# Performance work log

Hardware: AMD Instinct MI355X
Metric: run time of the kernel (lower is better)

## Reference

```python
import jax, jax.numpy as jnp
import numpy as np

N, E, H, F, G, L = 20000, 320000, 128, 128, 50, 6
CUTOFF = 5.0
LOG2 = 0.6931471805599453  # shift of ShiftedSoftplus
PI = np.pi


def ssp(x):
    # ShiftedSoftplus: softplus(x) - log(2)
    return jax.nn.softplus(x) - LOG2


def setup_inputs() -> dict:
    key = jax.random.key(0)
    ks = jax.random.split(key, 12)
    v = jax.random.normal(ks[0], (N, H), jnp.float32)
    pos = jax.random.uniform(ks[1], (N, 3), jnp.float32) * 2.0
    offsets_real = jax.random.normal(ks[2], (E, 3), jnp.float32) * 0.3
    edges = jax.random.randint(ks[3], (2, E), 0, N, jnp.int32)
    s = lambda k, shp, fan_in: jax.random.normal(k, shp, jnp.float32) / np.sqrt(fan_in)
    # update_e params (torch Linear weights stored as [in, out] for x @ W)
    lin_w = s(ks[4], (L, H, F), H)        # Linear(hidden, filters, bias=False)
    w1 = s(ks[5], (L, G, F), G)           # mlp[0]: Linear(gaussians, filters)
    b1 = jnp.zeros((L, F), jnp.float32)
    w2 = s(ks[6], (L, F, F), F)           # mlp[2]: Linear(filters, filters)
    b2 = jnp.zeros((L, F), jnp.float32)
    # update_v params
    u1 = s(ks[7], (L, F, H), F)           # lin1: Linear(filters, hidden)
    ub1 = jnp.zeros((L, H), jnp.float32)
    u2 = s(ks[8], (L, H, H), H)           # lin2: Linear(hidden, hidden)
    ub2 = jnp.zeros((L, H), jnp.float32)
    return {"v": v, "pos": pos, "offsets_real": offsets_real, "edges": edges,
            "lin_w": lin_w, "w1": w1, "b1": b1, "w2": w2, "b2": b2,
            "u1": u1, "ub1": ub1, "u2": u2, "ub2": ub2}


def reference(v, pos, offsets_real, edges, lin_w, w1, b1, w2, b2, u1, ub1, u2, ub2):
    row, col = edges[0], edges[1]
    # pairwise distances with periodic offsets: [E]
    diff = pos[col] + offsets_real - pos[row]
    dist = jnp.sqrt(jnp.sum(diff * diff, axis=-1))
    # Gaussian RBF expansion: [E, G]
    offset = jnp.linspace(0.0, CUTOFF, G)
    coeff = -0.5 / (offset[1] - offset[0]) ** 2
    demb = jnp.exp(coeff * (dist[:, None] - offset[None, :]) ** 2)
    # cosine cutoff envelope: [E]
    C = 0.5 * (jnp.cos(dist * PI / CUTOFF) + 1.0)
    for l in range(L):
        # continuous filter from RBFs: [E, F]
        Wf = (ssp(demb @ w1[l] + b1[l]) @ w2[l] + b2[l]) * C[:, None]
        # update_e: project nodes then gather source features
        e = (v @ lin_w[l])[row] * Wf                      # [E, F]
        # update_v: scatter-add messages to targets, residual MLP
        agg = jax.ops.segment_sum(e, col, num_segments=N)  # [N, F]
        out = ssp(agg @ u1[l] + ub1[l]) @ u2[l] + ub2[l]
        v = v + out
    return v
```

## Files before the change

kernel.cpp:

```cpp
#include <hip/hip_runtime.h>
#include <hip/hip_bf16.h>
#include <math.h>

#define HH 128
#define FF 128
#define GG 50
#define NLAYERS 6
#define NPB 16
#define TAB 4096
#define TABH 0.001953125f
#define TABINVH 512.0f
#define SCB 32
#define DP 8

typedef __attribute__((ext_vector_type(8))) short bf16x8;
typedef __attribute__((ext_vector_type(4))) float f32x4;

static __device__ __forceinline__ float ssp(float x) {
    return fmaxf(x, 0.f) + __logf(1.f + __expf(-fabsf(x))) - 0.6931471805599453f;
}

static __device__ __forceinline__ short f2bf(float x) {
    union { float f; unsigned u; } c; c.f = x;
    unsigned r = (c.u + 0x7FFF + ((c.u >> 16) & 1)) >> 16;
    return (short)r;
}

static __device__ __forceinline__ float bf2f_lo(unsigned p) {
    union { unsigned u; float f; } c; c.u = p << 16; return c.f;
}
static __device__ __forceinline__ float bf2f_hi(unsigned p) {
    union { unsigned u; float f; } c; c.u = p & 0xFFFF0000u; return c.f;
}

__global__ void hist_kernel(const int* __restrict__ col, int* __restrict__ counts, int E_) {
    int e = blockIdx.x * 256 + threadIdx.x;
    if (e < E_) atomicAdd(&counts[col[e]], 1);
}

__global__ __launch_bounds__(1024) void pscan1_kernel(const int* __restrict__ counts,
                                                      int* __restrict__ psum, int N_) {
    __shared__ int wsum[16];
    const int tid = threadIdx.x;
    const int lane = tid & 63, wid = tid >> 6;
    const int chunk = (N_ + SCB - 1) / SCB;
    int i = blockIdx.x * chunk + tid;
    int val = (tid < chunk && i < N_) ? counts[i] : 0;
#pragma unroll
    for (int d = 1; d < 64; d <<= 1) val += __shfl_xor(val, d, 64);
    if (lane == 0) wsum[wid] = val;
    __syncthreads();
    if (wid == 0) {
        int s = (lane < 16) ? wsum[lane] : 0;
#pragma unroll
        for (int d = 1; d < 16; d <<= 1) s += __shfl_xor(s, d, 64);
        if (lane == 0) psum[blockIdx.x] = s;
    }
}

__global__ void pscan2_kernel(const int* __restrict__ psum, int* __restrict__ pbase) {
    const int tid = threadIdx.x;
    int v = (tid < SCB) ? psum[tid] : 0;
    int x = v;
#pragma unroll
    for (int d = 1; d < 64; d <<= 1) {
        int t = __shfl_up(x, d, 64);
        if (tid >= d) x += t;
    }
    if (tid < SCB) pbase[tid] = x - v;
}

__global__ __launch_bounds__(1024) void pscan3_kernel(const int* __restrict__ counts,
                                                      const int* __restrict__ pbase,
                                                      int* __restrict__ offsets,
                                                      int* __restrict__ woff, int N_) {
    __shared__ int wsum[16];
    const int tid = threadIdx.x;
    const int lane = tid & 63, wid = tid >> 6;
    const int chunk = (N_ + SCB - 1) / SCB;
    int i = blockIdx.x * chunk + tid;
    int val = (tid < chunk && i < N_) ? counts[i] : 0;
    int x = val;
#pragma unroll
    for (int d = 1; d < 64; d <<= 1) {
        int t = __shfl_up(x, d, 64);
        if (lane >= d) x += t;
    }
    if (lane == 63) wsum[wid] = x;
    __syncthreads();
    if (wid == 0) {
        int s = (lane < 16) ? wsum[lane] : 0;
#pragma unroll
        for (int d = 1; d < 16; d <<= 1) {
            int t = __shfl_up(s, d, 64);
            if (lane >= d) s += t;
        }
        if (lane < 16) wsum[lane] = s;
    }
    __syncthreads();
    int woffset = (wid > 0) ? wsum[wid - 1] : 0;
    if (tid < chunk && i < N_) {
        int ex = pbase[blockIdx.x] + woffset + x - val;
        offsets[i] = ex;
        woff[i] = ex;
    }
}

__global__ void scatter_kernel(const float* __restrict__ pos,
                               const float* __restrict__ offs,
                               const int* __restrict__ row,
                               const int* __restrict__ col,
                               int* __restrict__ woff,
                               int2* __restrict__ meta, int E_) {
    int e = blockIdx.x * 256 + threadIdx.x;
    if (e >= E_) return;
    int r = row[e], c = col[e];
    float dx = pos[c * 3 + 0] + offs[e * 3 + 0] - pos[r * 3 + 0];
    float dy = pos[c * 3 + 1] + offs[e * 3 + 1] - pos[r * 3 + 1];
    float dz = pos[c * 3 + 2] + offs[e * 3 + 2] - pos[r * 3 + 2];
    float d = sqrtf(dx * dx + dy * dy + dz * dz);
    float x = d * TABINVH;
    int ix = (int)x;
    if (ix > TAB - 2) ix = TAB - 2;
    float fr = x - (float)ix;
    unsigned frb = (unsigned)(unsigned short)f2bf(fr);
    int p = atomicAdd(&woff[c], 1);
    meta[p] = make_int2(r, (int)((frb << 16) | (unsigned)ix));
}

__global__ __launch_bounds__(256) void prep_kernel(
    const float* __restrict__ w1, const float* __restrict__ w2,
    const float* __restrict__ u1, const float* __restrict__ u2,
    const float* __restrict__ lin_w,
    short* __restrict__ w1t, short* __restrict__ w2t,
    short* __restrict__ u1t, short* __restrict__ u2t, short* __restrict__ lin_wt) {
    int idx = blockIdx.x * 256 + threadIdx.x;
    if (idx < NLAYERS * FF * FF) {
        int l = idx >> 14, r = idx & 16383, a = r >> 7, b = r & 127;
        size_t src = (size_t)l * FF * FF + (size_t)b * FF + a;
        w2t[idx] = f2bf(w2[src]);
        u1t[idx] = f2bf(u1[src]);
        u2t[idx] = f2bf(u2[src]);
        lin_wt[idx] = f2bf(lin_w[src]);
    }
    if (idx < NLAYERS * FF * 64) {
        int l = idx >> 13, r = idx & 8191, fo = r >> 6, g = r & 63;
        w1t[idx] = f2bf(g < GG ? w1[((size_t)l * GG + g) * FF + fo] : 0.f);
    }
}

__global__ __launch_bounds__(256) void vproj0_kernel(const float* __restrict__ vb,
                                                     const short* __restrict__ lwt,
                                                     unsigned short* __restrict__ out,
                                                     int N_) {
    const int tid = threadIdx.x;
    const int lane = tid & 63, wave = tid >> 6;
    const int l15 = lane & 15, l4 = lane >> 4;
    const int n0 = wave * 32;
    const int nb0 = blockIdx.x * 64;
    bf16x8 bw[2][4];
#pragma unroll
    for (int n = 0; n < 2; n++)
#pragma unroll
        for (int ks = 0; ks < 4; ks++)
            bw[n][ks] = *(const bf16x8*)&lwt[(n0 + n * 16 + l15) * 128 + ks * 32 + l4 * 8];
#pragma unroll
    for (int m = 0; m < 4; m++) {
        f32x4 acc0 = {0.f, 0.f, 0.f, 0.f}, acc1 = {0.f, 0.f, 0.f, 0.f};
        int arow = nb0 + m * 16 + l15;
        const float* ap = &vb[(size_t)(arow < N_ ? arow : 0) * HH];
#pragma unroll
        for (int ks = 0; ks < 4; ks++) {
            float4 x0 = *(const float4*)&ap[ks * 32 + l4 * 8];
            float4 x1 = *(const float4*)&ap[ks * 32 + l4 * 8 + 4];
            bf16x8 a = {f2bf(x0.x), f2bf(x0.y), f2bf(x0.z), f2bf(x0.w),
                        f2bf(x1.x), f2bf(x1.y), f2bf(x1.z), f2bf(x1.w)};
            acc0 = __builtin_amdgcn_mfma_f32_16x16x32_bf16(a, bw[0][ks], acc0, 0, 0, 0);
            acc1 = __builtin_amdgcn_mfma_f32_16x16x32_bf16(a, bw[1][ks], acc1, 0, 0, 0);
        }
#pragma unroll
        for (int r = 0; r < 4; r++) {
            int gn = nb0 + m * 16 + l4 * 4 + r;
            if (gn < N_) {
                out[(size_t)gn * FF + n0 + l15] = (unsigned short)f2bf(acc0[r]);
                out[(size_t)gn * FF + n0 + 16 + l15] = (unsigned short)f2bf(acc1[r]);
            }
        }
    }
}

__global__ __launch_bounds__(256) void tab_kernel(
    const short* __restrict__ w1t, const float* __restrict__ b1,
    const short* __restrict__ w2t, const float* __restrict__ b2,
    unsigned short* __restrict__ tab) {
    __shared__ __align__(16) short h1_s[64 * 136];
    const int tid = threadIdx.x;
    const int lane = tid & 63, wave = tid >> 6;
    const int l15 = lane & 15, l4 = lane >> 4;
    const int n0w = wave * 32;
    const int l = blockIdx.x / (TAB / 64);
    const int tb0 = (blockIdx.x % (TAB / 64)) * 64;
    const short* w1l = w1t + (size_t)l * FF * 64;
    const short* w2l = w2t + (size_t)l * FF * FF;
    unsigned short* tabl = tab + (size_t)l * TAB * FF;

    bf16x8 bw1[2][2], bw2[2][4];
    float bias1[2], bias2[2];
#pragma unroll
    for (int n = 0; n < 2; n++) {
        const int fo = n0w + n * 16 + l15;
        bias1[n] = b1[(size_t)l * FF + fo];
        bias2[n] = b2[(size_t)l * FF + fo];
#pragma unroll
        for (int ks = 0; ks < 2; ks++)
            bw1[n][ks] = *(const bf16x8*)&w1l[fo * 64 + ks * 32 + l4 * 8];
#pragma unroll
        for (int ks = 0; ks < 4; ks++)
            bw2[n][ks] = *(const bf16x8*)&w2l[fo * 128 + ks * 32 + l4 * 8];
    }

    const float STEP = 5.0f / 49.0f;
    const float COEFF = -0.5f / (STEP * STEP);
#pragma unroll
    for (int m = 0; m < 4; m++) {
        float d = (float)(tb0 + m * 16 + l15) * TABH;
        bf16x8 a0, a1;
#pragma unroll
        for (int j = 0; j < 8; j++) {
            int g0 = l4 * 8 + j;
            float x0 = fmaf((float)g0, -STEP, d);
            a0[j] = f2bf(__expf(COEFF * x0 * x0));
            int g1 = 32 + l4 * 8 + j;
            float x1 = fmaf((float)g1, -STEP, d);
            a1[j] = (g1 < GG) ? f2bf(__expf(COEFF * x1 * x1)) : (short)0;
        }
#pragma unroll
        for (int n = 0; n < 2; n++) {
            f32x4 acc = {bias1[n], bias1[n], bias1[n], bias1[n]};
            acc = __builtin_amdgcn_mfma_f32_16x16x32_bf16(a0, bw1[n][0], acc, 0, 0, 0);
            acc = __builtin_amdgcn_mfma_f32_16x16x32_bf16(a1, bw1[n][1], acc, 0, 0, 0);
            const int f = n0w + n * 16 + l15;
#pragma unroll
            for (int r = 0; r < 4; r++)
                h1_s[(m * 16 + l4 * 4 + r) * 136 + f] = f2bf(ssp(acc[r]));
        }
    }
    __syncthreads();

#pragma unroll
    for (int m = 0; m < 4; m++) {
        f32x4 accA = {bias2[0], bias2[0], bias2[0], bias2[0]};
        f32x4 accB = {bias2[1], bias2[1], bias2[1], bias2[1]};
#pragma unroll
        for (int ks = 0; ks < 4; ks++) {
            bf16x8 a = *(const bf16x8*)&h1_s[(m * 16 + l15) * 136 + ks * 32 + l4 * 8];
            accA = __builtin_amdgcn_mfma_f32_16x16x32_bf16(a, bw2[0][ks], accA, 0, 0, 0);
            accB = __builtin_amdgcn_mfma_f32_16x16x32_bf16(a, bw2[1][ks], accB, 0, 0, 0);
        }
#pragma unroll
        for (int r = 0; r < 4; r++) {
            int entry = tb0 + m * 16 + l4 * 4 + r;
            float de = (float)entry * TABH;
            float C = 0.5f * (cosf(de * 0.6283185307179586f) + 1.0f);
            tabl[(size_t)entry * FF + n0w + l15] = (unsigned short)f2bf(accA[r] * C);
            tabl[(size_t)entry * FF + n0w + 16 + l15] = (unsigned short)f2bf(accB[r] * C);
        }
    }
}

__global__ __launch_bounds__(256) void repack_kernel(const unsigned short* __restrict__ tab,
                                                     int2* __restrict__ tabp) {
    int idx = blockIdx.x * 256 + threadIdx.x;
    if (idx >= NLAYERS * TAB * 64) return;
    int l = idx / (TAB * 64);
    int r = idx - l * (TAB * 64);
    int i = r >> 6, f2 = r & 63;
    const unsigned short* tl = tab + (size_t)l * TAB * FF;
    unsigned lo = *(const unsigned*)&tl[(size_t)i * FF + 2 * f2];
    unsigned hi = (i + 1 < TAB) ? *(const unsigned*)&tl[(size_t)(i + 1) * FF + 2 * f2] : lo;
    tabp[idx] = make_int2((int)lo, (int)hi);
}

__global__ __launch_bounds__(512) void layer_kernel(
    const int2* __restrict__ meta,
    const int* __restrict__ off_start, const int* __restrict__ off_end,
    const int2* __restrict__ tabp, const unsigned* __restrict__ vin,
    const short* __restrict__ u1t, const float* __restrict__ ub1,
    const short* __restrict__ u2t, const float* __restrict__ ub2,
    float* __restrict__ vb, const short* __restrict__ lwt_next,
    unsigned short* __restrict__ vout, int N_) {
    __shared__ __align__(16) float agg_s[NPB * 132];
    __shared__ __align__(16) short t1_s[NPB * 136];
    short* t2_s = (short*)agg_s;

    const int tid = threadIdx.x;
    const int lane = tid & 63, wave = tid >> 6;
    const int l15 = lane & 15, l4 = lane >> 4;
    const int n0c = wave * 16;
    const int nb0 = blockIdx.x * NPB;

#pragma unroll
    for (int s = 0; s < 2; s++) {
        const int nl = wave * 2 + s;
        const int n = nb0 + nl;
        float acc0 = 0.f, acc1 = 0.f;
        if (n < N_) {
            const int e0 = __builtin_amdgcn_readfirstlane(off_start[n]);
            const int e1 = __builtin_amdgcn_readfirstlane(off_end[n]);
            if (e1 > e0) {
                int2 mmn[DP];
#pragma unroll
                for (int j = 0; j < DP; j++) {
                    int e = e0 + j; if (e >= e1) e = e1 - 1;
                    mmn[j] = meta[e];
                }
                for (int base = e0; base < e1; base += DP) {
                    int rr[DP], ww[DP];
#pragma unroll
                    for (int j = 0; j < DP; j++) {
                        rr[j] = __builtin_amdgcn_readfirstlane(mmn[j].x);
                        ww[j] = __builtin_amdgcn_readfirstlane(mmn[j].y);
                    }
                    int2 tp[DP]; unsigned vp[DP];
#pragma unroll
                    for (int j = 0; j < DP; j++) {
                        tp[j] = tabp[(size_t)(ww[j] & 0xffff) * 64 + lane];
                        vp[j] = vin[(size_t)rr[j] * 64 + lane];
                    }
                    const int nb2 = base + DP;
                    if (nb2 < e1) {
#pragma unroll
                        for (int j = 0; j < DP; j++) {
                            int e = nb2 + j; if (e >= e1) e = e1 - 1;
                            mmn[j] = meta[e];
                        }
                    }
#pragma unroll
                    for (int j = 0; j < DP; j++) {
                        if (base + j < e1) {
                            const float fr = bf2f_hi((unsigned)ww[j]);
                            const float ta0 = bf2f_lo((unsigned)tp[j].x);
                            const float ta1 = bf2f_hi((unsigned)tp[j].x);
                            const float tb0 = bf2f_lo((unsigned)tp[j].y);
                            const float tb1 = bf2f_hi((unsigned)tp[j].y);
                            acc0 = fmaf(fmaf(fr, tb0 - ta0, ta0), bf2f_lo(vp[j]), acc0);
                            acc1 = fmaf(fmaf(fr, tb1 - ta1, ta1), bf2f_hi(vp[j]), acc1);
                        }
                    }
                }
            }
        }
        agg_s[nl * 132 + 2 * lane] = acc0;
        agg_s[nl * 132 + 2 * lane + 1] = acc1;
    }
    __syncthreads();

    {
        bf16x8 bw[4];
        const float bias = ub1[n0c + l15];
#pragma unroll
        for (int ks = 0; ks < 4; ks++)
            bw[ks] = *(const bf16x8*)&u1t[(n0c + l15) * 128 + ks * 32 + l4 * 8];
        const float* ap = &agg_s[l15 * 132];
        f32x4 acc = {bias, bias, bias, bias};
#pragma unroll
        for (int ks = 0; ks < 4; ks++) {
            float4 x0 = *(const float4*)&ap[ks * 32 + l4 * 8];
            float4 x1 = *(const float4*)&ap[ks * 32 + l4 * 8 + 4];
            bf16x8 a = {f2bf(x0.x), f2bf(x0.y), f2bf(x0.z), f2bf(x0.w),
                        f2bf(x1.x), f2bf(x1.y), f2bf(x1.z), f2bf(x1.w)};
            acc = __builtin_amdgcn_mfma_f32_16x16x32_bf16(a, bw[ks], acc, 0, 0, 0);
        }
#pragma unroll
        for (int r = 0; r < 4; r++) {
            int er = l4 * 4 + r;
            t1_s[er * 136 + n0c + l15] = f2bf(ssp(acc[r]));
        }
    }
    __syncthreads();

    {
        bf16x8 bw[4];
        const float bias = ub2[n0c + l15];
#pragma unroll
        for (int ks = 0; ks < 4; ks++)
            bw[ks] = *(const bf16x8*)&u2t[(n0c + l15) * 128 + ks * 32 + l4 * 8];
        f32x4 acc = {bias, bias, bias, bias};
#pragma unroll
        for (int ks = 0; ks < 4; ks++) {
            bf16x8 a = *(const bf16x8*)&t1_s[(l15) * 136 + ks * 32 + l4 * 8];
            acc = __builtin_amdgcn_mfma_f32_16x16x32_bf16(a, bw[ks], acc, 0, 0, 0);
        }
        __syncthreads();
#pragma unroll
        for (int r = 0; r < 4; r++) {
            int er = l4 * 4 + r;
            int gn = nb0 + er;
            if (gn < N_) {
                size_t i0 = (size_t)gn * HH + n0c + l15;
                float v0 = vb[i0] + acc[r];
                vb[i0] = v0;
                t2_s[er * 136 + n0c + l15] = f2bf(v0);
            } else {
                t2_s[er * 136 + n0c + l15] = 0;
            }
        }
    }
    __syncthreads();

    if (lwt_next) {
        bf16x8 bw[4];
#pragma unroll
        for (int ks = 0; ks < 4; ks++)
            bw[ks] = *(const bf16x8*)&lwt_next[(n0c + l15) * 128 + ks * 32 + l4 * 8];
        f32x4 acc = {0.f, 0.f, 0.f, 0.f};
#pragma unroll
        for (int ks = 0; ks < 4; ks++) {
            bf16x8 a = *(const bf16x8*)&t2_s[(l15) * 136 + ks * 32 + l4 * 8];
            acc = __builtin_amdgcn_mfma_f32_16x16x32_bf16(a, bw[ks], acc, 0, 0, 0);
        }
#pragma unroll
        for (int r = 0; r < 4; r++) {
            int gn = nb0 + l4 * 4 + r;
            if (gn < N_) {
                vout[(size_t)gn * FF + n0c + l15] = (unsigned short)f2bf(acc[r]);
            }
        }
    }
}

extern "C" void kernel_launch(void* const* d_in, const int* in_sizes, int n_in,
                              void* d_out, int out_size, void* d_ws, size_t ws_size,
                              hipStream_t stream) {
    const float* v = (const float*)d_in[0];
    const float* pos = (const float*)d_in[1];
    const float* offs = (const float*)d_in[2];
    const int* edges = (const int*)d_in[3];
    const float* lin_w = (const float*)d_in[4];
    const float* w1 = (const float*)d_in[5];
    const float* b1 = (const float*)d_in[6];
    const float* w2 = (const float*)d_in[7];
    const float* b2 = (const float*)d_in[8];
    const float* u1 = (const float*)d_in[9];
    const float* ub1 = (const float*)d_in[10];
    const float* u2 = (const float*)d_in[11];
    const float* ub2 = (const float*)d_in[12];

    const int N = in_sizes[0] / HH;
    const int E = in_sizes[3] / 2;
    const int* row = edges;
    const int* col = edges + E;

    char* base = (char*)d_ws;
    int* counts = (int*)base;    base += (size_t)N * 4;
    int* woff = (int*)base;      base += (size_t)N * 4;
    int* offsets = (int*)base;   base += (size_t)N * 4;
    int* psum = (int*)base;      base += (size_t)SCB * 4;
    int* pbase = (int*)base;     base += (size_t)SCB * 4 + 24;
    int2* meta = (int2*)base;    base += (size_t)E * 8;
    unsigned short* vprojA = (unsigned short*)base; base += (size_t)N * FF * 2;
    unsigned short* vprojB = (unsigned short*)base; base += (size_t)N * FF * 2;
    short* w1t = (short*)base;   base += (size_t)NLAYERS * FF * 64 * 2;
    short* w2t = (short*)base;   base += (size_t)NLAYERS * FF * FF * 2;
    short* u1t = (short*)base;   base += (size_t)NLAYERS * FF * FF * 2;
    short* u2t = (short*)base;   base += (size_t)NLAYERS * FF * FF * 2;
    short* lin_wt = (short*)base; base += (size_t)NLAYERS * FF * FF * 2;
    unsigned short* tab = (unsigned short*)base; base += (size_t)NLAYERS * TAB * FF * 2;
    int2* tabp = (int2*)base;

    float* vbuf = (float*)d_out;

    const int EB = (E + 255) / 256;
    const int NB64 = (N + 63) / 64;
    const int NBn = (N + NPB - 1) / NPB;

    hipMemsetAsync(counts, 0, (size_t)N * 4, stream);
    hist_kernel<<<EB, 256, 0, stream>>>(col, counts, E);
    pscan1_kernel<<<SCB, 1024, 0, stream>>>(counts, psum, N);
    pscan2_kernel<<<1, 64, 0, stream>>>(psum, pbase);
    pscan3_kernel<<<SCB, 1024, 0, stream>>>(counts, pbase, offsets, woff, N);
    scatter_kernel<<<EB, 256, 0, stream>>>(pos, offs, row, col, woff, meta, E);
    prep_kernel<<<(NLAYERS * FF * FF + 255) / 256, 256, 0, stream>>>(
        w1, w2, u1, u2, lin_w, w1t, w2t, u1t, u2t, lin_wt);
    tab_kernel<<<NLAYERS * (TAB / 64), 256, 0, stream>>>(w1t, b1, w2t, b2, tab);
    repack_kernel<<<(NLAYERS * TAB * 64 + 255) / 256, 256, 0, stream>>>(tab, tabp);
    hipMemcpyAsync(vbuf, v, (size_t)N * HH * sizeof(float),
                   hipMemcpyDeviceToDevice, stream);
    vproj0_kernel<<<NB64, 256, 0, stream>>>(v, lin_wt, vprojA, N);

    for (int l = 0; l < NLAYERS; l++) {
        unsigned short* vin = (l & 1) ? vprojB : vprojA;
        unsigned short* vout = (l & 1) ? vprojA : vprojB;
        layer_kernel<<<NBn, 512, 0, stream>>>(
            meta, offsets, woff, tabp + (size_t)l * TAB * 64, (const unsigned*)vin,
            u1t + (size_t)l * FF * FF, ub1 + (size_t)l * HH,
            u2t + (size_t)l * FF * FF, ub2 + (size_t)l * HH, vbuf,
            (l + 1 < NLAYERS) ? (lin_wt + (size_t)(l + 1) * FF * FF) : nullptr,
            vout, N);
    }
}
```

Measured before the change: 310.2 us.

## Replace interpolated filter table with finer nearest-neighbor table and packed edge metadata

The filter lookup table grows 4x finer and uses nearest-entry lookup in place of linear interpolation. This removes the repack kernel and halves the per-edge table load from an int2 pair to one 32-bit word. Edge metadata is packed into a single int (17-bit row index plus table index), which halves metadata traffic, and the gather prefetch depth doubles. In exchange, the table build does 4x more MFMA work, the table gets larger and is less cache-friendly, and nearest-neighbor lookup adds some approximation error. The 17-bit row packing also assumes N stays below 131072.

```diff
diff --git a/kernel.cpp b/kernel.cpp
--- a/kernel.cpp
+++ b/kernel.cpp
@@ -7,11 +7,11 @@
 #define GG 50
 #define NLAYERS 6
 #define NPB 16
-#define TAB 4096
-#define TABH 0.001953125f
-#define TABINVH 512.0f
+#define TAB 16384
+#define TABH 4.8828125e-4f
+#define TABINVH 2048.0f
 #define SCB 32
-#define DP 8
+#define DP 16
 
 typedef __attribute__((ext_vector_type(8))) short bf16x8;
 typedef __attribute__((ext_vector_type(4))) float f32x4;
@@ -111,7 +111,7 @@
                                const int* __restrict__ row,
                                const int* __restrict__ col,
                                int* __restrict__ woff,
-                               int2* __restrict__ meta, int E_) {
+                               int* __restrict__ meta, int E_) {
     int e = blockIdx.x * 256 + threadIdx.x;
     if (e >= E_) return;
     int r = row[e], c = col[e];
@@ -119,13 +119,10 @@
     float dy = pos[c * 3 + 1] + offs[e * 3 + 1] - pos[r * 3 + 1];
     float dz = pos[c * 3 + 2] + offs[e * 3 + 2] - pos[r * 3 + 2];
     float d = sqrtf(dx * dx + dy * dy + dz * dz);
-    float x = d * TABINVH;
-    int ix = (int)x;
-    if (ix > TAB - 2) ix = TAB - 2;
-    float fr = x - (float)ix;
-    unsigned frb = (unsigned)(unsigned short)f2bf(fr);
+    int ix = (int)(d * TABINVH + 0.5f);
+    if (ix > TAB - 1) ix = TAB - 1;
     int p = atomicAdd(&woff[c], 1);
-    meta[p] = make_int2(r, (int)((frb << 16) | (unsigned)ix));
+    meta[p] = r | (ix << 17);
 }
 
 __global__ __launch_bounds__(256) void prep_kernel(
@@ -268,23 +265,10 @@
     }
 }
 
-__global__ __launch_bounds__(256) void repack_kernel(const unsigned short* __restrict__ tab,
-                                                     int2* __restrict__ tabp) {
-    int idx = blockIdx.x * 256 + threadIdx.x;
-    if (idx >= NLAYERS * TAB * 64) return;
-    int l = idx / (TAB * 64);
-    int r = idx - l * (TAB * 64);
-    int i = r >> 6, f2 = r & 63;
-    const unsigned short* tl = tab + (size_t)l * TAB * FF;
-    unsigned lo = *(const unsigned*)&tl[(size_t)i * FF + 2 * f2];
-    unsigned hi = (i + 1 < TAB) ? *(const unsigned*)&tl[(size_t)(i + 1) * FF + 2 * f2] : lo;
-    tabp[idx] = make_int2((int)lo, (int)hi);
-}
-
 __global__ __launch_bounds__(512) void layer_kernel(
-    const int2* __restrict__ meta,
+    const int* __restrict__ meta,
     const int* __restrict__ off_start, const int* __restrict__ off_end,
-    const int2* __restrict__ tabp, const unsigned* __restrict__ vin,
+    const unsigned* __restrict__ tab, const unsigned* __restrict__ vin,
     const short* __restrict__ u1t, const float* __restrict__ ub1,
     const short* __restrict__ u2t, const float* __restrict__ ub2,
     float* __restrict__ vb, const short* __restrict__ lwt_next,
@@ -308,24 +292,24 @@
             const int e0 = __builtin_amdgcn_readfirstlane(off_start[n]);
             const int e1 = __builtin_amdgcn_readfirstlane(off_end[n]);
             if (e1 > e0) {
-                int2 mmn[DP];
+                int mmn[DP];
 #pragma unroll
                 for (int j = 0; j < DP; j++) {
                     int e = e0 + j; if (e >= e1) e = e1 - 1;
                     mmn[j] = meta[e];
                 }
                 for (int base = e0; base < e1; base += DP) {
-                    int rr[DP], ww[DP];
+                    int mw[DP];
+#pragma unroll
+                    for (int j = 0; j < DP; j++)
+                        mw[j] = __builtin_amdgcn_readfirstlane(mmn[j]);
+                    unsigned tp[DP], vp[DP];
 #pragma unroll
                     for (int j = 0; j < DP; j++) {
-                        rr[j] = __builtin_amdgcn_readfirstlane(mmn[j].x);
-                        ww[j] = __builtin_amdgcn_readfirstlane(mmn[j].y);
-                    }
-                    int2 tp[DP]; unsigned vp[DP];
-#pragma unroll
-                    for (int j = 0; j < DP; j++) {
-                        tp[j] = tabp[(size_t)(ww[j] & 0xffff) * 64 + lane];
-                        vp[j] = vin[(size_t)rr[j] * 64 + lane];
+                        const int r_ = mw[j] & 0x1ffff;
+                        const int ix = (int)((unsigned)mw[j] >> 17);
+                        tp[j] = tab[(size_t)ix * 64 + lane];
+                        vp[j] = vin[(size_t)r_ * 64 + lane];
                     }
                     const int nb2 = base + DP;
                     if (nb2 < e1) {
@@ -338,13 +322,8 @@
 #pragma unroll
                     for (int j = 0; j < DP; j++) {
                         if (base + j < e1) {
-                            const float fr = bf2f_hi((unsigned)ww[j]);
-                            const float ta0 = bf2f_lo((unsigned)tp[j].x);
-                            const float ta1 = bf2f_hi((unsigned)tp[j].x);
-                            const float tb0 = bf2f_lo((unsigned)tp[j].y);
-                            const float tb1 = bf2f_hi((unsigned)tp[j].y);
-                            acc0 = fmaf(fmaf(fr, tb0 - ta0, ta0), bf2f_lo(vp[j]), acc0);
-                            acc1 = fmaf(fmaf(fr, tb1 - ta1, ta1), bf2f_hi(vp[j]), acc1);
+                            acc0 = fmaf(bf2f_lo(tp[j]), bf2f_lo(vp[j]), acc0);
+                            acc1 = fmaf(bf2f_hi(tp[j]), bf2f_hi(vp[j]), acc1);
                         }
                     }
                 }
@@ -457,7 +436,7 @@
     int* offsets = (int*)base;   base += (size_t)N * 4;
     int* psum = (int*)base;      base += (size_t)SCB * 4;
     int* pbase = (int*)base;     base += (size_t)SCB * 4 + 24;
-    int2* meta = (int2*)base;    base += (size_t)E * 8;
+    int* meta = (int*)base;      base += (size_t)E * 4;
     unsigned short* vprojA = (unsigned short*)base; base += (size_t)N * FF * 2;
     unsigned short* vprojB = (unsigned short*)base; base += (size_t)N * FF * 2;
     short* w1t = (short*)base;   base += (size_t)NLAYERS * FF * 64 * 2;
@@ -465,8 +444,7 @@
     short* u1t = (short*)base;   base += (size_t)NLAYERS * FF * FF * 2;
     short* u2t = (short*)base;   base += (size_t)NLAYERS * FF * FF * 2;
     short* lin_wt = (short*)base; base += (size_t)NLAYERS * FF * FF * 2;
-    unsigned short* tab = (unsigned short*)base; base += (size_t)NLAYERS * TAB * FF * 2;
-    int2* tabp = (int2*)base;
+    unsigned short* tab = (unsigned short*)base;
 
     float* vbuf = (float*)d_out;
 
@@ -483,7 +461,6 @@
     prep_kernel<<<(NLAYERS * FF * FF + 255) / 256, 256, 0, stream>>>(
         w1, w2, u1, u2, lin_w, w1t, w2t, u1t, u2t, lin_wt);
     tab_kernel<<<NLAYERS * (TAB / 64), 256, 0, stream>>>(w1t, b1, w2t, b2, tab);
-    repack_kernel<<<(NLAYERS * TAB * 64 + 255) / 256, 256, 0, stream>>>(tab, tabp);
     hipMemcpyAsync(vbuf, v, (size_t)N * HH * sizeof(float),
                    hipMemcpyDeviceToDevice, stream);
     vproj0_kernel<<<NB64, 256, 0, stream>>>(v, lin_wt, vprojA, N);
@@ -492,7 +469,8 @@
         unsigned short* vin = (l & 1) ? vprojB : vprojA;
         unsigned short* vout = (l & 1) ? vprojA : vprojB;
         layer_kernel<<<NBn, 512, 0, stream>>>(
-            meta, offsets, woff, tabp + (size_t)l * TAB * 64, (const unsigned*)vin,
+            meta, offsets, woff, (const unsigned*)(tab + (size_t)l * TAB * FF),
+            (const unsigned*)vin,
             u1t + (size_t)l * FF * FF, ub1 + (size_t)l * HH,
             u2t + (size_t)l * FF * FF, ub2 + (size_t)l * HH, vbuf,
             (l + 1 < NLAYERS) ? (lin_wt + (size_t)(l + 1) * FF * FF) : nullptr,
```

Result: faster. 302.1 us (-2.6%).
